# Performance work log

Measured on AMD Instinct MI355X. Metric: run time of the kernel, lower is better.

Reference implementation:

```python
import jax, jax.numpy as jnp
import numpy as np

B, N, E_PER = 512, 256, 8192          # graphs, nodes per graph, edges per graph
FIN, H, K, FOUT = 128, 32, 16, 10     # in_channels, hidden, num clusters, out_channels
EPS = 1e-15


def setup_inputs() -> dict:
    key = jax.random.key(0)
    ks = jax.random.split(key, 12)
    x = jax.random.normal(ks[0], (B * N, FIN), jnp.float32)
    # intra-graph random edges, then offset into the global node index space
    src = jax.random.randint(ks[1], (B, E_PER), 0, N)
    dst = jax.random.randint(ks[2], (B, E_PER), 0, N)
    offs = (jnp.arange(B) * N)[:, None]
    edge_index = jnp.stack([(src + offs).reshape(-1), (dst + offs).reshape(-1)]).astype(jnp.int64)
    batch = jnp.repeat(jnp.arange(B), N).astype(jnp.int64)

    def lin(k, fin, fout):
        return (jax.random.normal(k, (fin, fout), jnp.float32) / np.sqrt(fin)).astype(jnp.float32)

    params = {
        'W_lin1': lin(ks[3], FIN, H), 'b_lin1': jnp.zeros((H,), jnp.float32),
        'W_rel1': lin(ks[4], H, H), 'b_rel1': jnp.zeros((H,), jnp.float32),
        'W_root1': lin(ks[5], H, H),
        'W_pool': lin(ks[6], H, K), 'b_pool': jnp.zeros((K,), jnp.float32),
        'W_rel2': lin(ks[7], H, H), 'b_rel2': jnp.zeros((H,), jnp.float32),
        'W_root2': lin(ks[8], H, H),
        'W_lin2': lin(ks[9], H, H), 'b_lin2': jnp.zeros((H,), jnp.float32),
        'W_lin3': lin(ks[10], H, FOUT), 'b_lin3': jnp.zeros((FOUT,), jnp.float32),
    }
    return {'x': x, 'edge_index': edge_index, 'batch': batch, **params}


def _densify(x, edge_index, batch):
    """to_dense_adj + to_dense_batch: [total,F] -> [B,N,F], [B,N,N], [B,N]."""
    n_total = x.shape[0]
    counts = jax.ops.segment_sum(jnp.ones((n_total,), jnp.int32), batch, num_segments=B)
    offsets = jnp.concatenate([jnp.zeros((1,), jnp.int32), jnp.cumsum(counts)[:-1]])
    pos = jnp.arange(n_total) - offsets[batch]            # position of node inside its graph
    eb = batch[edge_index[0]]                             # graph id of each edge
    adj = jnp.zeros((B, N, N), jnp.float32).at[eb, pos[edge_index[0]], pos[edge_index[1]]].add(1.0)
    xd = jnp.zeros((B, N, x.shape[1]), jnp.float32).at[batch, pos].set(x)
    mask = jnp.zeros((B, N), jnp.float32).at[batch, pos].set(1.0)
    return xd, adj, mask


def _dense_graph_conv(x, adj, W_rel, b_rel, W_root):
    # PyG DenseGraphConv(aggr='add'): lin_rel(adj @ x) + lin_root(x)
    return jnp.einsum('bnm,bmh,hk->bnk', adj, x, W_rel) + b_rel + x @ W_root


def _dense_mincut_pool(x, adj, s, mask):
    s = jax.nn.softmax(s, axis=-1)
    x = x * mask[..., None]
    s = s * mask[..., None]
    out = jnp.einsum('bnk,bnh->bkh', s, x)                        # s^T x
    out_adj = jnp.einsum('bnk,bnm,bmj->bkj', s, adj, s)           # s^T A s
    mincut_num = jnp.einsum('bkk->b', out_adj)
    d_flat = adj.sum(-1)                                          # degree
    mincut_den = jnp.einsum('bnk,bn,bnk->b', s, d_flat, s)        # trace(s^T D s)
    mincut_loss = jnp.mean(-(mincut_num / mincut_den))
    ss = jnp.einsum('bnk,bnj->bkj', s, s)
    ss_norm = jnp.linalg.norm(ss, axis=(-1, -2), keepdims=True)
    i_s = jnp.eye(K, dtype=jnp.float32)
    ortho_loss = jnp.mean(jnp.linalg.norm(ss / ss_norm - i_s / jnp.sqrt(jnp.float32(K)), axis=(-1, -2)))
    # zero diagonal, symmetric degree normalization
    diag_mask = 1.0 - i_s
    out_adj = out_adj * diag_mask
    d = jnp.sqrt(out_adj.sum(-1))[:, None, :] + EPS               # [B,1,K]
    out_adj = out_adj / d / jnp.swapaxes(d, 1, 2)
    return out, out_adj, mincut_loss, ortho_loss


def reference(x, edge_index, batch, W_lin1, b_lin1, W_rel1, b_rel1, W_root1,
              W_pool, b_pool, W_rel2, b_rel2, W_root2, W_lin2, b_lin2, W_lin3, b_lin3):
    xd, adj, mask = _densify(x, edge_index, batch)
    h = xd @ W_lin1 + b_lin1                                      # lin1
    h = _dense_graph_conv(h, adj, W_rel1, b_rel1, W_root1)        # conv1
    s2 = h @ W_pool + b_pool                                      # pool2
    h, adj_p, mincut_loss2, ortho_loss2 = _dense_mincut_pool(h, adj, s2, mask)
    h = _dense_graph_conv(h, adj_p, W_rel2, b_rel2, W_root2)      # conv2
    h = h.sum(axis=1)                                             # readout sum over clusters
    h = jax.nn.relu(h @ W_lin2 + b_lin2)
    h = h @ W_lin3 + b_lin3
    return jax.nn.log_softmax(h, axis=-1), mincut_loss2, ortho_loss2
```

## Files before the change

kernel.cpp:

```cpp
#include <hip/hip_runtime.h>

#define NB 512
#define NN 256
#define EPG 8192
#define FINC 128

typedef float f32x4 __attribute__((ext_vector_type(4)));
typedef short s16x8 __attribute__((ext_vector_type(8)));

__device__ __forceinline__ float bf2f(unsigned short u) {
  union { unsigned int i; float f; } x; x.i = ((unsigned int)u) << 16; return x.f;
}
__device__ __forceinline__ unsigned short f2bf(float f) {
  union { float f; unsigned int i; } x; x.f = f;
  unsigned int r = x.i + 0x7fffu + ((x.i >> 16) & 1u);
  return (unsigned short)(r >> 16);
}
__device__ __forceinline__ unsigned pk2(unsigned short a, unsigned short c) {
  return (unsigned)a | ((unsigned)c << 16);
}

union U16x8 { uint4 u; s16x8 s; };
__device__ __forceinline__ s16x8 dec8(unsigned d) {
  U16x8 o;
  o.u.x = 0x41804180u | ((d & 0x0000000Fu) << 3)  | ((d & 0x000000F0u) << 15);
  o.u.y = 0x41804180u | ((d & 0x00000F00u) >> 5)  | ((d & 0x0000F000u) << 7);
  o.u.z = 0x41804180u | ((d & 0x000F0000u) >> 13) | ((d & 0x00F00000u) >> 1);
  o.u.w = 0x41804180u | ((d & 0x0F000000u) >> 21) | ((d & 0xF0000000u) >> 9);
  return o.s;
}

struct Params {
  const void* x; const void* ei;
  const void *wl1, *bl1, *wr1, *br1, *wro1, *wp, *bp;
  const void *wr2, *br2, *wro2, *wl2, *bl2, *wl3, *bl3;
  float* out; float* ws;
};

__device__ __forceinline__ bool detect_bf16(const void* p) {
  const unsigned short* pw = (const unsigned short*)p;
  int sane = 0;
  for (int i = 0; i < 64; ++i) {
    unsigned e = (pw[i] >> 7) & 0xFFu;
    sane += (e > 96u && e < 132u) ? 1 : 0;
  }
  return sane >= 56;
}
__device__ __forceinline__ bool detect_i64(const void* p) {
  const int* pi = (const int*)p + EPG;
  int ok = 0;
  for (int i = 0; i < 32; ++i) ok += (pi[i] >= 256 && pi[i] < 512) ? 1 : 0;
  return ok < 24;
}
__device__ __forceinline__ float ldf(const void* p, int i, bool bf) {
  return bf ? bf2f(((const unsigned short*)p)[i]) : ((const float*)p)[i];
}

#define SMEM_TOTAL 81920

__global__ __launch_bounds__(1024, 8) void mincut_main(Params P) {
  extern __shared__ char smem[];
  const int t = threadIdx.x;
  const int b = blockIdx.x;

  const bool BF  = detect_bf16(P.wr1);
  const bool I64 = detect_i64(P.ei);

  float* pbuf   = (float*)(smem + 0);
  float* oadjb  = (float*)(smem + 2048);
  float* ssb    = (float*)(smem + 3072);
  float* qbuf   = (float*)(smem + 4096);
  float* ddb    = (float*)(smem + 6144);
  float* h2b    = (float*)(smem + 6208);
  float* rb     = (float*)(smem + 8256);
  float* yb     = (float*)(smem + 8384);
  float* lgb    = (float*)(smem + 8512);
  float* scr    = (float*)(smem + 8704);
  float* rel2f  = (float*)(smem + 9216);
  float* root2f = (float*)(smem + 13312);
  float* lin2f  = (float*)(smem + 17408);
  float* lin3f  = (float*)(smem + 21504);
  float* brel2f = (float*)(smem + 22784);
  float* blin2f = (float*)(smem + 22912);
  float* blin3f = (float*)(smem + 23040);
  float* pbufH  = (float*)(smem + 24576);
  float* pbufL  = (float*)(smem + 26624);
  float* oadjH  = (float*)(smem + 28672);
  float* oadjL  = (float*)(smem + 29696);
  float* ssA    = (float*)(smem + 30720);
  float* ssX    = (float*)(smem + 31744);
  unsigned short* h0T  = (unsigned short*)(smem + 33792);
  unsigned short* h1Th = (unsigned short*)(smem + 33792);
  unsigned short* w1t  = (unsigned short*)(smem + 50688);
  unsigned short* zT   = (unsigned short*)(smem + 50688);
  unsigned short* sTh  = (unsigned short*)(smem + 50688);
  unsigned short* sTl  = (unsigned short*)(smem + 59136);
  unsigned short* wrelTh = (unsigned short*)(smem + 67584);
  unsigned short* wrelTl = (unsigned short*)(smem + 70144);
  unsigned short* wrootT = (unsigned short*)(smem + 72704);
  float* blin1f = (float*)(smem + 75264);
  unsigned short* taT = (unsigned short*)(smem + 67584);
  unsigned short* wpoolTh = (unsigned short*)(smem + 76032);
  unsigned short* wpoolTl = (unsigned short*)(smem + 77184);
  float*          colzF   = (float*)(smem + 78336);
  float*          colsF   = (float*)(smem + 78464);
  float*          scrE    = (float*)(smem + 78528);
  float*          bpf     = (float*)(smem + 78592);
  unsigned short* brel1h  = (unsigned short*)(smem + 81856);

  const int wv = t >> 6, lane = t & 63;
  const int lm = lane & 15, quad = lane >> 4;
  const int mbase = wv * 16;

  {
    uint4 z = {0u, 0u, 0u, 0u};
    for (int i = t; i < 2112; i += 1024) ((uint4*)smem)[i] = z;
  }
  if (t < 48) colzF[t] = 0.f;
  for (int e = t; e < 4096; e += 1024) {
    int k = e >> 5, c = e & 31;
    w1t[c * 136 + k] = f2bf(ldf(P.wl1, e, BF));
  }
  {
    int k = t >> 5, c = t & 31;
    float wr = ldf(P.wr1, t, BF);
    unsigned short hi = f2bf(wr);
    wrelTh[c * 40 + k] = hi;
    wrelTl[c * 40 + k] = f2bf(wr - bf2f(hi));
    wrootT[c * 40 + k] = f2bf(ldf(P.wro1, t, BF));
  }
  if (t < 512) {
    int m = t >> 4, c = t & 15;
    float w = ldf(P.wp, t, BF);
    unsigned short hi = f2bf(w);
    wpoolTh[c * 36 + m] = hi;
    wpoolTl[c * 36 + m] = f2bf(w - bf2f(hi));
  }
  if (t < 32) { blin1f[t] = ldf(P.bl1, t, BF); brel1h[t] = f2bf(ldf(P.br1, t, BF)); }
  if (t < 16) bpf[t] = ldf(P.bp, t, BF);
  __syncthreads();

  if (I64) {
    const uint4* s4 = (const uint4*)((const long long*)P.ei + (size_t)b * EPG) + t * 4;
    const uint4* d4 = (const uint4*)((const long long*)P.ei + (size_t)NB * EPG + (size_t)b * EPG) + t * 4;
    #pragma unroll
    for (int i = 0; i < 4; ++i) {
      uint4 a = s4[i], c = d4[i];
      unsigned n0 = (a.x & 255u) * 264u + (c.x & 255u);
      unsigned n1 = (a.z & 255u) * 264u + (c.z & 255u);
      atomicAdd((unsigned int*)(smem + ((n0 >> 3) << 2)), 1u << ((n0 & 7u) * 4u));
      atomicAdd((unsigned int*)(smem + ((n1 >> 3) << 2)), 1u << ((n1 & 7u) * 4u));
    }
  } else {
    const uint4* s4 = (const uint4*)((const int*)P.ei + (size_t)b * EPG) + t * 2;
    const uint4* d4 = (const uint4*)((const int*)P.ei + (size_t)NB * EPG + (size_t)b * EPG) + t * 2;
    #pragma unroll
    for (int i = 0; i < 2; ++i) {
      uint4 a = s4[i], c = d4[i];
      unsigned n0 = (a.x & 255u) * 264u + (c.x & 255u);
      unsigned n1 = (a.y & 255u) * 264u + (c.y & 255u);
      unsigned n2 = (a.z & 255u) * 264u + (c.z & 255u);
      unsigned n3 = (a.w & 255u) * 264u + (c.w & 255u);
      atomicAdd((unsigned int*)(smem + ((n0 >> 3) << 2)), 1u << ((n0 & 7u) * 4u));
      atomicAdd((unsigned int*)(smem + ((n1 >> 3) << 2)), 1u << ((n1 & 7u) * 4u));
      atomicAdd((unsigned int*)(smem + ((n2 >> 3) << 2)), 1u << ((n2 & 7u) * 4u));
      atomicAdd((unsigned int*)(smem + ((n3 >> 3) << 2)), 1u << ((n3 & 7u) * 4u));
    }
  }

  {
    f32x4 acc[2] = {{0.f,0.f,0.f,0.f},{0.f,0.f,0.f,0.f}};
    const size_t node = (size_t)(b * 256 + mbase + lm);
    #pragma unroll
    for (int ks = 0; ks < 4; ++ks) {
      const int k0 = ks * 32 + quad * 8;
      s16x8 a;
      if (BF) {
        a = *(const s16x8*)((const unsigned short*)P.x + node * 128 + k0);
      } else {
        const float* xp = (const float*)P.x + node * 128 + k0;
        f32x4 v0 = *(const f32x4*)xp;
        f32x4 v1 = *(const f32x4*)(xp + 4);
        #pragma unroll
        for (int j = 0; j < 4; ++j) { a[j] = (short)f2bf(v0[j]); a[4 + j] = (short)f2bf(v1[j]); }
      }
      #pragma unroll
      for (int ct = 0; ct < 2; ++ct) {
        s16x8 bh = *(const s16x8*)(w1t + (ct * 16 + lm) * 136 + k0);
        acc[ct] = __builtin_amdgcn_mfma_f32_16x16x32_bf16(a, bh, acc[ct], 0, 0, 0);
      }
    }
    #pragma unroll
    for (int ct = 0; ct < 2; ++ct) {
      const int c = ct * 16 + lm;
      float bias = blin1f[c];
      *(uint2*)(h0T + c * 264 + mbase + quad * 4) =
          make_uint2(pk2(f2bf(acc[ct][0] + bias), f2bf(acc[ct][1] + bias)),
                     pk2(f2bf(acc[ct][2] + bias), f2bf(acc[ct][3] + bias)));
    }
  }
  __syncthreads();

  f32x4 racc[2] = {{0.f,0.f,0.f,0.f},{0.f,0.f,0.f,0.f}};
  {
    s16x8 Ah;
    #pragma unroll
    for (int j = 0; j < 8; ++j) Ah[j] = (short)h0T[(quad * 8 + j) * 264 + mbase + lm];
    f32x4 zacc[2] = {{0.f,0.f,0.f,0.f},{0.f,0.f,0.f,0.f}};
    #pragma unroll
    for (int ct = 0; ct < 2; ++ct) {
      const int c = ct * 16 + lm;
      s16x8 brh = *(const s16x8*)(wrelTh + c * 40 + quad * 8);
      s16x8 brl = *(const s16x8*)(wrelTl + c * 40 + quad * 8);
      s16x8 bro = *(const s16x8*)(wrootT + c * 40 + quad * 8);
      zacc[ct] = __builtin_amdgcn_mfma_f32_16x16x32_bf16(Ah, brh, zacc[ct], 0, 0, 0);
      zacc[ct] = __builtin_amdgcn_mfma_f32_16x16x32_bf16(Ah, brl, zacc[ct], 0, 0, 0);
      racc[ct] = __builtin_amdgcn_mfma_f32_16x16x32_bf16(Ah, bro, racc[ct], 0, 0, 0);
    }
    #pragma unroll
    for (int ct = 0; ct < 2; ++ct) {
      unsigned short u0 = f2bf(zacc[ct][0]), u1 = f2bf(zacc[ct][1]);
      unsigned short u2 = f2bf(zacc[ct][2]), u3 = f2bf(zacc[ct][3]);
      *(uint2*)(zT + (ct * 16 + lm) * 264 + mbase + quad * 4) =
          make_uint2(pk2(u0, u1), pk2(u2, u3));
      float pz = (bf2f(u0) + bf2f(u1)) + (bf2f(u2) + bf2f(u3));
      pz += __shfl_xor(pz, 16, 64);
      pz += __shfl_xor(pz, 32, 64);
      if (lane < 16) atomicAdd(colzF + ct * 16 + lm, pz);
    }
  }
  __syncthreads();

  float degf;
  {
    f32x4 h1acc[2] = { racc[0], racc[1] };
    unsigned dsum = 0;
    const char* arow = smem + (mbase + lm) * 132;
    #pragma unroll
    for (int ks = 0; ks < 8; ++ks) {
      unsigned d = *(const unsigned int*)(arow + ks * 16 + quad * 4);
      unsigned v = (d & 0x0F0F0F0Fu) + ((d >> 4) & 0x0F0F0F0Fu);
      dsum += (v * 0x01010101u) >> 24;
      s16x8 af = dec8(d);
      const int v0 = ks * 32 + quad * 8;
      #pragma unroll
      for (int ct = 0; ct < 2; ++ct) {
        s16x8 bz = *(const s16x8*)(zT + (ct * 16 + lm) * 264 + v0);
        h1acc[ct] = __builtin_amdgcn_mfma_f32_16x16x32_bf16(af, bz, h1acc[ct], 0, 0, 0);
      }
    }
    dsum += __shfl_xor(dsum, 16, 64);
    dsum += __shfl_xor(dsum, 32, 64);
    degf = (float)dsum;
    #pragma unroll
    for (int ct = 0; ct < 2; ++ct) {
      const int c = ct * 16 + lm;
      float bias = bf2f(brel1h[c]) - 16.f * colzF[c];
      *(uint2*)(h1Th + c * 264 + mbase + quad * 4) =
          make_uint2(pk2(f2bf(h1acc[ct][0] + bias), f2bf(h1acc[ct][1] + bias)),
                     pk2(f2bf(h1acc[ct][2] + bias), f2bf(h1acc[ct][3] + bias)));
    }
  }
  __syncthreads();

  {
    s16x8 Ah1;
    #pragma unroll
    for (int j = 0; j < 8; ++j) Ah1[j] = (short)h1Th[(quad * 8 + j) * 264 + mbase + lm];
    s16x8 Bh, Bl;
    ((uint2*)&Bh)[0] = *(const uint2*)(wpoolTh + lm * 36 + quad * 8);
    ((uint2*)&Bh)[1] = *(const uint2*)(wpoolTh + lm * 36 + quad * 8 + 4);
    ((uint2*)&Bl)[0] = *(const uint2*)(wpoolTl + lm * 36 + quad * 8);
    ((uint2*)&Bl)[1] = *(const uint2*)(wpoolTl + lm * 36 + quad * 8 + 4);
    f32x4 lacc = {0.f, 0.f, 0.f, 0.f};
    lacc = __builtin_amdgcn_mfma_f32_16x16x32_bf16(Ah1, Bh, lacc, 0, 0, 0);
    lacc = __builtin_amdgcn_mfma_f32_16x16x32_bf16(Ah1, Bl, lacc, 0, 0, 0);
    f32x4 lg;
    float bm = bpf[lm];
    #pragma unroll
    for (int r = 0; r < 4; ++r) lg[r] = lacc[r] + bm;
    f32x4 mx = lg;
    #pragma unroll
    for (int m = 1; m <= 8; m <<= 1)
      #pragma unroll
      for (int r = 0; r < 4; ++r) mx[r] = fmaxf(mx[r], __shfl_xor(mx[r], m, 64));
    #pragma unroll
    for (int r = 0; r < 4; ++r) lg[r] = __expf(lg[r] - mx[r]);
    f32x4 sm = lg;
    #pragma unroll
    for (int m = 1; m <= 8; m <<= 1)
      #pragma unroll
      for (int r = 0; r < 4; ++r) sm[r] += __shfl_xor(sm[r], m, 64);
    f32x4 sval, sq;
    #pragma unroll
    for (int r = 0; r < 4; ++r) { sval[r] = lg[r] / sm[r]; sq[r] = sval[r] * sval[r]; }
    #pragma unroll
    for (int m = 1; m <= 8; m <<= 1)
      #pragma unroll
      for (int r = 0; r < 4; ++r) sq[r] += __shfl_xor(sq[r], m, 64);
    {
      unsigned short h0s = f2bf(sval[0]); float r0 = bf2f(h0s); unsigned short l0 = f2bf(sval[0] - r0);
      unsigned short h1s = f2bf(sval[1]); float r1 = bf2f(h1s); unsigned short l1 = f2bf(sval[1] - r1);
      unsigned short h2s = f2bf(sval[2]); float r2 = bf2f(h2s); unsigned short l2 = f2bf(sval[2] - r2);
      unsigned short h3s = f2bf(sval[3]); float r3 = bf2f(h3s); unsigned short l3 = f2bf(sval[3] - r3);
      const int nb = lm * 264 + mbase + quad * 4;
      *(uint2*)(sTh + nb) = make_uint2(pk2(h0s, h1s), pk2(h2s, h3s));
      *(uint2*)(sTl + nb) = make_uint2(pk2(l0, l1), pk2(l2, l3));
      float sr = ((r0 + bf2f(l0)) + (r1 + bf2f(l1))) + ((r2 + bf2f(l2)) + (r3 + bf2f(l3)));
      sr += __shfl_xor(sr, 16, 64);
      sr += __shfl_xor(sr, 32, 64);
      if (lane < 16) atomicAdd(colsF + lm, sr);
    }
    {
      int l = lane & 15, src = (l >> 2) << 4;
      float q0 = __shfl(sq[0], src, 64), q1 = __shfl(sq[1], src, 64);
      float q2 = __shfl(sq[2], src, 64), q3 = __shfl(sq[3], src, 64);
      float ssel = (l & 2) ? ((l & 1) ? q3 : q2) : ((l & 1) ? q1 : q0);
      float vden = (lane < 16) ? degf * ssel : 0.f;
      #pragma unroll
      for (int o = 32; o > 0; o >>= 1) vden += __shfl_xor(vden, o, 64);
      if (lane == 0) scrE[wv] = vden;
    }
  }
  __syncthreads();

  {
    float cols = colsF[lm];
    f32x4 tacc = {0.f, 0.f, 0.f, 0.f};
    const char* arow = smem + (mbase + lm) * 132;
    #pragma unroll
    for (int ks = 0; ks < 8; ++ks) {
      unsigned d = *(const unsigned int*)(arow + ks * 16 + quad * 4);
      s16x8 af = dec8(d);
      const int v0 = ks * 32 + quad * 8;
      s16x8 bh = *(const s16x8*)(sTh + lm * 264 + v0);
      s16x8 bl = *(const s16x8*)(sTl + lm * 264 + v0);
      tacc = __builtin_amdgcn_mfma_f32_16x16x32_bf16(af, bh, tacc, 0, 0, 0);
      tacc = __builtin_amdgcn_mfma_f32_16x16x32_bf16(af, bl, tacc, 0, 0, 0);
    }
    float c16 = 16.f * cols;
    *(uint2*)(taT + lm * 264 + mbase + quad * 4) =
        make_uint2(pk2(f2bf(tacc[0] - c16), f2bf(tacc[1] - c16)),
                   pk2(f2bf(tacc[2] - c16), f2bf(tacc[3] - c16)));
  }
  __syncthreads();

  rel2f[t] = ldf(P.wr2, t, BF);
  root2f[t] = ldf(P.wro2, t, BF);
  lin2f[t] = ldf(P.wl2, t, BF);
  if (t < 320) lin3f[t] = ldf(P.wl3, t, BF);
  if (t < 32) brel2f[t] = ldf(P.br2, t, BF);
  if (t < 32) blin2f[t] = ldf(P.bl2, t, BF);
  if (t < 10) blin3f[t] = ldf(P.bl3, t, BF);

  if (wv < 8) {
    const unsigned short *Ap, *Bp; float* dst; int W, ct = 0;
    switch (wv) {
      case 0: Ap = sTh; Bp = h1Th; dst = pbufH; W = 32; ct = 0; break;
      case 1: Ap = sTh; Bp = h1Th; dst = pbufH; W = 32; ct = 1; break;
      case 2: Ap = sTl; Bp = h1Th; dst = pbufL; W = 32; ct = 0; break;
      case 3: Ap = sTl; Bp = h1Th; dst = pbufL; W = 32; ct = 1; break;
      case 4: Ap = sTh; Bp = taT;  dst = oadjH; W = 16; break;
      case 5: Ap = sTl; Bp = taT;  dst = oadjL; W = 16; break;
      case 6: Ap = sTh; Bp = sTh;  dst = ssA;   W = 16; break;
      default: Ap = sTh; Bp = sTl; dst = ssX;   W = 16; break;
    }
    const int cidx = ct * 16 + lm;
    const unsigned short* Bb = Bp + cidx * 264;
    f32x4 acc = {0.f, 0.f, 0.f, 0.f};
    #pragma unroll
    for (int ch = 0; ch < 8; ++ch) {
      s16x8 a = *(const s16x8*)(Ap + lm * 264 + ch * 32 + quad * 8);
      s16x8 bb = *(const s16x8*)(Bb + ch * 32 + quad * 8);
      acc = __builtin_amdgcn_mfma_f32_16x16x32_bf16(a, bb, acc, 0, 0, 0);
    }
    #pragma unroll
    for (int r = 0; r < 4; ++r) dst[(quad * 4 + r) * W + cidx] = acc[r];
  }
  __syncthreads();

  if (t < 512) {
    pbuf[t] = pbufH[t] + pbufL[t];
  } else if (t < 768) {
    int i = t - 512; oadjb[i] = oadjH[i] + oadjL[i];
  } else {
    int i = t - 768; int k3 = i >> 4, j3 = i & 15;
    ssb[i] = ssA[i] + ssX[i] + ssX[j3 * 16 + k3];
  }
  __syncthreads();

  {
    float vnum = (t < 16) ? oadjb[t * 17] : 0.f;
    float vfro = (t < 256) ? ssb[t] * ssb[t] : 0.f;
    float vtr  = (t < 16) ? ssb[t * 17] : 0.f;
    #pragma unroll
    for (int o = 32; o > 0; o >>= 1) {
      vnum += __shfl_xor(vnum, o, 64);
      vfro += __shfl_xor(vfro, o, 64);
      vtr  += __shfl_xor(vtr, o, 64);
    }
    if (lane == 0) { scr[16 + wv] = vnum; scr[32 + wv] = vfro; scr[48 + wv] = vtr; }
  }
  __syncthreads();

  if (t == 0) {
    float den = 0.f, num = 0.f, fro = 0.f, tr = 0.f;
    #pragma unroll
    for (int i = 0; i < 16; ++i) { den += scrE[i]; num += scr[16 + i]; fro += scr[32 + i]; tr += scr[48 + i]; }
    float ssn = sqrtf(fro);
    float orth2 = 2.f - tr / (2.f * ssn);
    atomicAdd(P.ws, -(num / den) * (1.f / NB));
    atomicAdd(P.ws + 1, sqrtf(fmaxf(orth2, 0.f)) * (1.f / NB));
  }
  if (t < 16) {
    float rs = 0.f;
    #pragma unroll
    for (int j = 0; j < 16; ++j) if (j != t) rs += oadjb[t * 16 + j];
    ddb[t] = sqrtf(rs) + 1e-15f;
  }
  __syncthreads();
  if (t < 256) {
    int k = t >> 4, j = t & 15;
    float apv = (k == j) ? 0.f : oadjb[t] / (ddb[k] * ddb[j]);
    oadjb[t] = apv;
  }
  __syncthreads();

  if (t < 512) {
    int k = t >> 5, c = t & 31;
    float q = 0.f;
    #pragma unroll
    for (int j = 0; j < 16; ++j) q += oadjb[k * 16 + j] * pbuf[j * 32 + c];
    qbuf[k * 32 + c] = q;
  }
  __syncthreads();
  if (t < 512) {
    int k = t >> 5, c = t & 31;
    float s0 = 0.f;
    #pragma unroll
    for (int m = 0; m < 32; ++m)
      s0 += qbuf[k * 32 + m] * rel2f[m * 32 + c] + pbuf[k * 32 + m] * root2f[m * 32 + c];
    h2b[k * 32 + c] = s0;
  }
  __syncthreads();

  if (wv == 0) {
    if (lane < 32) {
      float r = 16.f * brel2f[lane];
      #pragma unroll
      for (int k = 0; k < 16; ++k) r += h2b[k * 32 + lane];
      rb[lane] = r;
    }
    if (lane < 32) {
      float y = blin2f[lane];
      #pragma unroll
      for (int m = 0; m < 32; ++m) y += rb[m] * lin2f[m * 32 + lane];
      yb[lane] = fmaxf(y, 0.f);
    }
    if (lane < 10) {
      float lg = blin3f[lane];
      #pragma unroll
      for (int m = 0; m < 32; ++m) lg += yb[m] * lin3f[m * 10 + lane];
      lgb[lane] = lg;
    }
    if (lane == 0) {
      float mx = lgb[0];
      #pragma unroll
      for (int i = 1; i < 10; ++i) mx = fmaxf(mx, lgb[i]);
      float sum = 0.f;
      #pragma unroll
      for (int i = 0; i < 10; ++i) sum += __expf(lgb[i] - mx);
      lgb[10] = mx + __logf(sum);
    }
    if (lane < 10) {
      float val = lgb[lane] - lgb[10];
      if (BF) ((unsigned short*)P.out)[b * 10 + lane] = f2bf(val);
      else    P.out[b * 10 + lane] = val;
    }
  }
}

__global__ void mincut_fin(Params P) {
  if (threadIdx.x == 0) {
    const bool BF = detect_bf16(P.wr1);
    if (BF) {
      ((unsigned short*)P.out)[5120] = f2bf(P.ws[0]);
      ((unsigned short*)P.out)[5121] = f2bf(P.ws[1]);
    } else {
      P.out[5120] = P.ws[0];
      P.out[5121] = P.ws[1];
    }
  }
}

extern "C" void kernel_launch(void* const* d_in, const int* in_sizes, int n_in,
                              void* d_out, int out_size, void* d_ws, size_t ws_size,
                              hipStream_t stream) {
  (void)in_sizes; (void)n_in; (void)out_size; (void)ws_size;
  Params P;
  P.x    = d_in[0];
  P.ei   = d_in[1];
  P.wl1  = d_in[3];
  P.bl1  = d_in[4];
  P.wr1  = d_in[5];
  P.br1  = d_in[6];
  P.wro1 = d_in[7];
  P.wp   = d_in[8];
  P.bp   = d_in[9];
  P.wr2  = d_in[10];
  P.br2  = d_in[11];
  P.wro2 = d_in[12];
  P.wl2  = d_in[13];
  P.bl2  = d_in[14];
  P.wl3  = d_in[15];
  P.bl3  = d_in[16];
  P.out  = (float*)d_out;
  P.ws   = (float*)d_ws;

  hipMemsetAsync(d_ws, 0, 2 * sizeof(float), stream);
  hipFuncSetAttribute(reinterpret_cast<const void*>(mincut_main),
                      hipFuncAttributeMaxDynamicSharedMemorySize, SMEM_TOTAL);
  hipLaunchKernelGGL(mincut_main, dim3(NB), dim3(1024), SMEM_TOTAL, stream, P);
  hipLaunchKernelGGL(mincut_fin, dim3(1), dim3(64), 0, stream, P);
}
```

Before: 170.1 us.

## Fold lin1 into conv1 weights and collapse pooled tail into single-wave reductions

```diff
diff --git a/kernel.cpp b/kernel.cpp
--- a/kernel.cpp
+++ b/kernel.cpp
@@ -66,16 +66,14 @@
   const bool BF  = detect_bf16(P.wr1);
   const bool I64 = detect_i64(P.ei);
 
-  float* pbuf   = (float*)(smem + 0);
   float* oadjb  = (float*)(smem + 2048);
-  float* ssb    = (float*)(smem + 3072);
-  float* qbuf   = (float*)(smem + 4096);
   float* ddb    = (float*)(smem + 6144);
-  float* h2b    = (float*)(smem + 6208);
+  float* caf    = (float*)(smem + 6208);
+  float* psf    = (float*)(smem + 6272);
+  float* qsf    = (float*)(smem + 6400);
   float* rb     = (float*)(smem + 8256);
   float* yb     = (float*)(smem + 8384);
   float* lgb    = (float*)(smem + 8512);
-  float* scr    = (float*)(smem + 8704);
   float* rel2f  = (float*)(smem + 9216);
   float* root2f = (float*)(smem + 13312);
   float* lin2f  = (float*)(smem + 17408);
@@ -89,24 +87,28 @@
   float* oadjL  = (float*)(smem + 29696);
   float* ssA    = (float*)(smem + 30720);
   float* ssX    = (float*)(smem + 31744);
-  unsigned short* h0T  = (unsigned short*)(smem + 33792);
-  unsigned short* h1Th = (unsigned short*)(smem + 33792);
-  unsigned short* w1t  = (unsigned short*)(smem + 50688);
-  unsigned short* zT   = (unsigned short*)(smem + 50688);
-  unsigned short* sTh  = (unsigned short*)(smem + 50688);
-  unsigned short* sTl  = (unsigned short*)(smem + 59136);
-  unsigned short* wrelTh = (unsigned short*)(smem + 67584);
-  unsigned short* wrelTl = (unsigned short*)(smem + 70144);
-  unsigned short* wrootT = (unsigned short*)(smem + 72704);
-  float* blin1f = (float*)(smem + 75264);
-  unsigned short* taT = (unsigned short*)(smem + 67584);
+  unsigned short* M_relTh = (unsigned short*)(smem + 33792);
+  unsigned short* M_relTl = (unsigned short*)(smem + 42240);
+  unsigned short* h1Th    = (unsigned short*)(smem + 33792);
+  unsigned short* w1t    = (unsigned short*)(smem + 50688);
+  unsigned short* wrelTh = (unsigned short*)(smem + 59392);
+  unsigned short* wrelTl = (unsigned short*)(smem + 61952);
+  unsigned short* wrootT = (unsigned short*)(smem + 64512);
+  float*          blin1f = (float*)(smem + 67072);
+  unsigned short* zT     = (unsigned short*)(smem + 50688);
+  unsigned short* sTh    = (unsigned short*)(smem + 50688);
+  unsigned short* sTl    = (unsigned short*)(smem + 59136);
+  unsigned short* M_rootTh = (unsigned short*)(smem + 67584);
+  unsigned short* taT      = (unsigned short*)(smem + 67584);
   unsigned short* wpoolTh = (unsigned short*)(smem + 76032);
   unsigned short* wpoolTl = (unsigned short*)(smem + 77184);
   float*          colzF   = (float*)(smem + 78336);
   float*          colsF   = (float*)(smem + 78464);
   float*          scrE    = (float*)(smem + 78528);
   float*          bpf     = (float*)(smem + 78592);
-  unsigned short* brel1h  = (unsigned short*)(smem + 81856);
+  float*          bzf     = (float*)(smem + 78656);
+  float*          brf     = (float*)(smem + 78784);
+  float*          brel1f  = (float*)(smem + 78912);
 
   const int wv = t >> 6, lane = t & 63;
   const int lm = lane & 15, quad = lane >> 4;
@@ -136,9 +138,28 @@
     wpoolTh[c * 36 + m] = hi;
     wpoolTl[c * 36 + m] = f2bf(w - bf2f(hi));
   }
-  if (t < 32) { blin1f[t] = ldf(P.bl1, t, BF); brel1h[t] = f2bf(ldf(P.br1, t, BF)); }
+  if (t < 32) { blin1f[t] = ldf(P.bl1, t, BF); brel1f[t] = ldf(P.br1, t, BF); }
   if (t < 16) bpf[t] = ldf(P.bp, t, BF);
   __syncthreads();
+
+  s16x8 xa[4];
+  {
+    const size_t node = (size_t)(b * 256 + mbase + lm);
+    if (BF) {
+      #pragma unroll
+      for (int ks = 0; ks < 4; ++ks)
+        xa[ks] = *(const s16x8*)((const unsigned short*)P.x + node * 128 + ks * 32 + quad * 8);
+    } else {
+      #pragma unroll
+      for (int ks = 0; ks < 4; ++ks) {
+        const float* xp = (const float*)P.x + node * 128 + ks * 32 + quad * 8;
+        f32x4 v0 = *(const f32x4*)xp;
+        f32x4 v1 = *(const f32x4*)(xp + 4);
+        #pragma unroll
+        for (int j = 0; j < 4; ++j) { xa[ks][j] = (short)f2bf(v0[j]); xa[ks][4 + j] = (short)f2bf(v1[j]); }
+      }
+    }
+  }
 
   if (I64) {
     const uint4* s4 = (const uint4*)((const long long*)P.ei + (size_t)b * EPG) + t * 4;
@@ -169,64 +190,75 @@
   }
 
   {
-    f32x4 acc[2] = {{0.f,0.f,0.f,0.f},{0.f,0.f,0.f,0.f}};
-    const size_t node = (size_t)(b * 256 + mbase + lm);
+    const int mt = wv & 7, ct2 = wv >> 3;
+    const int c = ct2 * 16 + lm;
+    s16x8 Aw;
+    #pragma unroll
+    for (int j = 0; j < 8; ++j)
+      Aw[j] = (short)w1t[(quad * 8 + j) * 136 + mt * 16 + lm];
+    s16x8 Brh = *(const s16x8*)(wrelTh + c * 40 + quad * 8);
+    s16x8 Brl = *(const s16x8*)(wrelTl + c * 40 + quad * 8);
+    s16x8 Bro = *(const s16x8*)(wrootT + c * 40 + quad * 8);
+    f32x4 mr = {0.f,0.f,0.f,0.f}, mo = {0.f,0.f,0.f,0.f};
+    mr = __builtin_amdgcn_mfma_f32_16x16x32_bf16(Aw, Brh, mr, 0, 0, 0);
+    mr = __builtin_amdgcn_mfma_f32_16x16x32_bf16(Aw, Brl, mr, 0, 0, 0);
+    mo = __builtin_amdgcn_mfma_f32_16x16x32_bf16(Aw, Bro, mo, 0, 0, 0);
+    unsigned short h0_ = f2bf(mr[0]), h1_ = f2bf(mr[1]);
+    unsigned short h2_ = f2bf(mr[2]), h3_ = f2bf(mr[3]);
+    const int base = c * 132 + mt * 16 + quad * 4;
+    *(uint2*)(M_relTh + base) = make_uint2(pk2(h0_, h1_), pk2(h2_, h3_));
+    *(uint2*)(M_relTl + base) = make_uint2(
+        pk2(f2bf(mr[0] - bf2f(h0_)), f2bf(mr[1] - bf2f(h1_))),
+        pk2(f2bf(mr[2] - bf2f(h2_)), f2bf(mr[3] - bf2f(h3_))));
+    *(uint2*)(M_rootTh + base) = make_uint2(
+        pk2(f2bf(mo[0]), f2bf(mo[1])), pk2(f2bf(mo[2]), f2bf(mo[3])));
+  }
+  if (wv == 0) {
+    if (lane < 32) {
+      float s = 0.f;
+      #pragma unroll 8
+      for (int m = 0; m < 32; ++m)
+        s += blin1f[m] * (bf2f(wrelTh[lane * 40 + m]) + bf2f(wrelTl[lane * 40 + m]));
+      bzf[lane] = s;
+    } else {
+      int c = lane - 32;
+      float s = brel1f[c];
+      #pragma unroll 8
+      for (int m = 0; m < 32; ++m)
+        s += blin1f[m] * bf2f(wrootT[c * 40 + m]);
+      brf[c] = s;
+    }
+  }
+  __syncthreads();
+
+  f32x4 racc[2] = {{0.f,0.f,0.f,0.f},{0.f,0.f,0.f,0.f}};
+  {
+    f32x4 zacc[2] = {{0.f,0.f,0.f,0.f},{0.f,0.f,0.f,0.f}};
     #pragma unroll
     for (int ks = 0; ks < 4; ++ks) {
       const int k0 = ks * 32 + quad * 8;
-      s16x8 a;
-      if (BF) {
-        a = *(const s16x8*)((const unsigned short*)P.x + node * 128 + k0);
-      } else {
-        const float* xp = (const float*)P.x + node * 128 + k0;
-        f32x4 v0 = *(const f32x4*)xp;
-        f32x4 v1 = *(const f32x4*)(xp + 4);
-        #pragma unroll
-        for (int j = 0; j < 4; ++j) { a[j] = (short)f2bf(v0[j]); a[4 + j] = (short)f2bf(v1[j]); }
-      }
       #pragma unroll
       for (int ct = 0; ct < 2; ++ct) {
-        s16x8 bh = *(const s16x8*)(w1t + (ct * 16 + lm) * 136 + k0);
-        acc[ct] = __builtin_amdgcn_mfma_f32_16x16x32_bf16(a, bh, acc[ct], 0, 0, 0);
+        const int c = ct * 16 + lm;
+        s16x8 bzh = *(const s16x8*)(M_relTh + c * 132 + k0);
+        s16x8 bzl = *(const s16x8*)(M_relTl + c * 132 + k0);
+        s16x8 bro = *(const s16x8*)(M_rootTh + c * 132 + k0);
+        zacc[ct] = __builtin_amdgcn_mfma_f32_16x16x32_bf16(xa[ks], bzh, zacc[ct], 0, 0, 0);
+        zacc[ct] = __builtin_amdgcn_mfma_f32_16x16x32_bf16(xa[ks], bzl, zacc[ct], 0, 0, 0);
+        racc[ct] = __builtin_amdgcn_mfma_f32_16x16x32_bf16(xa[ks], bro, racc[ct], 0, 0, 0);
       }
     }
     #pragma unroll
     for (int ct = 0; ct < 2; ++ct) {
       const int c = ct * 16 + lm;
-      float bias = blin1f[c];
-      *(uint2*)(h0T + c * 264 + mbase + quad * 4) =
-          make_uint2(pk2(f2bf(acc[ct][0] + bias), f2bf(acc[ct][1] + bias)),
-                     pk2(f2bf(acc[ct][2] + bias), f2bf(acc[ct][3] + bias)));
-    }
-  }
-  __syncthreads();
-
-  f32x4 racc[2] = {{0.f,0.f,0.f,0.f},{0.f,0.f,0.f,0.f}};
-  {
-    s16x8 Ah;
-    #pragma unroll
-    for (int j = 0; j < 8; ++j) Ah[j] = (short)h0T[(quad * 8 + j) * 264 + mbase + lm];
-    f32x4 zacc[2] = {{0.f,0.f,0.f,0.f},{0.f,0.f,0.f,0.f}};
-    #pragma unroll
-    for (int ct = 0; ct < 2; ++ct) {
-      const int c = ct * 16 + lm;
-      s16x8 brh = *(const s16x8*)(wrelTh + c * 40 + quad * 8);
-      s16x8 brl = *(const s16x8*)(wrelTl + c * 40 + quad * 8);
-      s16x8 bro = *(const s16x8*)(wrootT + c * 40 + quad * 8);
-      zacc[ct] = __builtin_amdgcn_mfma_f32_16x16x32_bf16(Ah, brh, zacc[ct], 0, 0, 0);
-      zacc[ct] = __builtin_amdgcn_mfma_f32_16x16x32_bf16(Ah, brl, zacc[ct], 0, 0, 0);
-      racc[ct] = __builtin_amdgcn_mfma_f32_16x16x32_bf16(Ah, bro, racc[ct], 0, 0, 0);
-    }
-    #pragma unroll
-    for (int ct = 0; ct < 2; ++ct) {
-      unsigned short u0 = f2bf(zacc[ct][0]), u1 = f2bf(zacc[ct][1]);
-      unsigned short u2 = f2bf(zacc[ct][2]), u3 = f2bf(zacc[ct][3]);
-      *(uint2*)(zT + (ct * 16 + lm) * 264 + mbase + quad * 4) =
-          make_uint2(pk2(u0, u1), pk2(u2, u3));
+      float bz = bzf[c];
+      unsigned short u0 = f2bf(zacc[ct][0] + bz), u1 = f2bf(zacc[ct][1] + bz);
+      unsigned short u2 = f2bf(zacc[ct][2] + bz), u3 = f2bf(zacc[ct][3] + bz);
+      *(uint2*)(zT + c * 264 + mbase + quad * 4) = make_uint2(pk2(u0, u1), pk2(u2, u3));
       float pz = (bf2f(u0) + bf2f(u1)) + (bf2f(u2) + bf2f(u3));
       pz += __shfl_xor(pz, 16, 64);
       pz += __shfl_xor(pz, 32, 64);
-      if (lane < 16) atomicAdd(colzF + ct * 16 + lm, pz);
+      if (lane < 16) atomicAdd(colzF + c, pz);
     }
   }
   __syncthreads();
@@ -255,7 +287,7 @@
     #pragma unroll
     for (int ct = 0; ct < 2; ++ct) {
       const int c = ct * 16 + lm;
-      float bias = bf2f(brel1h[c]) - 16.f * colzF[c];
+      float bias = brf[c] - 16.f * colzF[c];
       *(uint2*)(h1Th + c * 264 + mbase + quad * 4) =
           make_uint2(pk2(f2bf(h1acc[ct][0] + bias), f2bf(h1acc[ct][1] + bias)),
                      pk2(f2bf(h1acc[ct][2] + bias), f2bf(h1acc[ct][3] + bias)));
@@ -353,7 +385,7 @@
   if (t < 32) blin2f[t] = ldf(P.bl2, t, BF);
   if (t < 10) blin3f[t] = ldf(P.bl3, t, BF);
 
-  if (wv < 8) {
+  {
     const unsigned short *Ap, *Bp; float* dst; int W, ct = 0;
     switch (wv) {
       case 0: Ap = sTh; Bp = h1Th; dst = pbufH; W = 32; ct = 0; break;
@@ -365,90 +397,57 @@
       case 6: Ap = sTh; Bp = sTh;  dst = ssA;   W = 16; break;
       default: Ap = sTh; Bp = sTl; dst = ssX;   W = 16; break;
     }
-    const int cidx = ct * 16 + lm;
-    const unsigned short* Bb = Bp + cidx * 264;
-    f32x4 acc = {0.f, 0.f, 0.f, 0.f};
-    #pragma unroll
-    for (int ch = 0; ch < 8; ++ch) {
-      s16x8 a = *(const s16x8*)(Ap + lm * 264 + ch * 32 + quad * 8);
-      s16x8 bb = *(const s16x8*)(Bb + ch * 32 + quad * 8);
-      acc = __builtin_amdgcn_mfma_f32_16x16x32_bf16(a, bb, acc, 0, 0, 0);
-    }
-    #pragma unroll
-    for (int r = 0; r < 4; ++r) dst[(quad * 4 + r) * W + cidx] = acc[r];
-  }
-  __syncthreads();
-
-  if (t < 512) {
-    pbuf[t] = pbufH[t] + pbufL[t];
-  } else if (t < 768) {
-    int i = t - 512; oadjb[i] = oadjH[i] + oadjL[i];
-  } else {
-    int i = t - 768; int k3 = i >> 4, j3 = i & 15;
-    ssb[i] = ssA[i] + ssX[i] + ssX[j3 * 16 + k3];
-  }
-  __syncthreads();
-
-  {
-    float vnum = (t < 16) ? oadjb[t * 17] : 0.f;
-    float vfro = (t < 256) ? ssb[t] * ssb[t] : 0.f;
-    float vtr  = (t < 16) ? ssb[t * 17] : 0.f;
-    #pragma unroll
-    for (int o = 32; o > 0; o >>= 1) {
-      vnum += __shfl_xor(vnum, o, 64);
-      vfro += __shfl_xor(vfro, o, 64);
-      vtr  += __shfl_xor(vtr, o, 64);
-    }
-    if (lane == 0) { scr[16 + wv] = vnum; scr[32 + wv] = vfro; scr[48 + wv] = vtr; }
-  }
-  __syncthreads();
-
-  if (t == 0) {
-    float den = 0.f, num = 0.f, fro = 0.f, tr = 0.f;
-    #pragma unroll
-    for (int i = 0; i < 16; ++i) { den += scrE[i]; num += scr[16 + i]; fro += scr[32 + i]; tr += scr[48 + i]; }
-    float ssn = sqrtf(fro);
-    float orth2 = 2.f - tr / (2.f * ssn);
-    atomicAdd(P.ws, -(num / den) * (1.f / NB));
-    atomicAdd(P.ws + 1, sqrtf(fmaxf(orth2, 0.f)) * (1.f / NB));
-  }
-  if (t < 16) {
-    float rs = 0.f;
-    #pragma unroll
-    for (int j = 0; j < 16; ++j) if (j != t) rs += oadjb[t * 16 + j];
-    ddb[t] = sqrtf(rs) + 1e-15f;
-  }
-  __syncthreads();
-  if (t < 256) {
-    int k = t >> 4, j = t & 15;
-    float apv = (k == j) ? 0.f : oadjb[t] / (ddb[k] * ddb[j]);
-    oadjb[t] = apv;
-  }
-  __syncthreads();
-
-  if (t < 512) {
-    int k = t >> 5, c = t & 31;
-    float q = 0.f;
-    #pragma unroll
-    for (int j = 0; j < 16; ++j) q += oadjb[k * 16 + j] * pbuf[j * 32 + c];
-    qbuf[k * 32 + c] = q;
-  }
-  __syncthreads();
-  if (t < 512) {
-    int k = t >> 5, c = t & 31;
-    float s0 = 0.f;
-    #pragma unroll
-    for (int m = 0; m < 32; ++m)
-      s0 += qbuf[k * 32 + m] * rel2f[m * 32 + c] + pbuf[k * 32 + m] * root2f[m * 32 + c];
-    h2b[k * 32 + c] = s0;
+    if (wv < 8) {
+      const int cidx = ct * 16 + lm;
+      const unsigned short* Bb = Bp + cidx * 264;
+      f32x4 acc = {0.f, 0.f, 0.f, 0.f};
+      #pragma unroll
+      for (int ch = 0; ch < 8; ++ch) {
+        s16x8 a = *(const s16x8*)(Ap + lm * 264 + ch * 32 + quad * 8);
+        s16x8 bb = *(const s16x8*)(Bb + ch * 32 + quad * 8);
+        acc = __builtin_amdgcn_mfma_f32_16x16x32_bf16(a, bb, acc, 0, 0, 0);
+      }
+      #pragma unroll
+      for (int r = 0; r < 4; ++r) dst[(quad * 4 + r) * W + cidx] = acc[r];
+    }
   }
   __syncthreads();
 
   if (wv == 0) {
+    #pragma unroll
+    for (int u = 0; u < 4; ++u) {
+      int i = lane * 4 + u;
+      oadjb[i] = oadjH[i] + oadjL[i];
+    }
+    if (lane < 16) {
+      float rs = 0.f;
+      #pragma unroll
+      for (int j = 0; j < 16; ++j) if (j != lane) rs += oadjb[lane * 16 + j];
+      ddb[lane] = sqrtf(rs) + 1e-15f;
+    }
+    if (lane < 16) {
+      float s = 0.f;
+      float dj = ddb[lane];
+      #pragma unroll
+      for (int k = 0; k < 16; ++k)
+        if (k != lane) s += oadjb[k * 16 + lane] / (ddb[k] * dj);
+      caf[lane] = s;
+    }
+    if (lane < 32) {
+      float ps = 0.f, qs = 0.f;
+      #pragma unroll
+      for (int j = 0; j < 16; ++j) {
+        float pv = pbufH[j * 32 + lane] + pbufL[j * 32 + lane];
+        ps += pv;
+        qs += caf[j] * pv;
+      }
+      psf[lane] = ps; qsf[lane] = qs;
+    }
     if (lane < 32) {
       float r = 16.f * brel2f[lane];
       #pragma unroll
-      for (int k = 0; k < 16; ++k) r += h2b[k * 32 + lane];
+      for (int m = 0; m < 32; ++m)
+        r += qsf[m] * rel2f[m * 32 + lane] + psf[m] * root2f[m * 32 + lane];
       rb[lane] = r;
     }
     if (lane < 32) {
@@ -476,6 +475,30 @@
       float val = lgb[lane] - lgb[10];
       if (BF) ((unsigned short*)P.out)[b * 10 + lane] = f2bf(val);
       else    P.out[b * 10 + lane] = val;
+    }
+  } else if (wv == 1) {
+    float vfro = 0.f, vtr = 0.f;
+    #pragma unroll
+    for (int u = 0; u < 4; ++u) {
+      int i = lane * 4 + u, k = i >> 4, j = i & 15;
+      float ssv = ssA[i] + ssX[i] + ssX[j * 16 + k];
+      vfro += ssv * ssv;
+      if (k == j) vtr += ssv;
+    }
+    float vnum = (lane < 16) ? (oadjH[lane * 17] + oadjL[lane * 17]) : 0.f;
+    float vden = (lane < 16) ? scrE[lane] : 0.f;
+    #pragma unroll
+    for (int o = 32; o > 0; o >>= 1) {
+      vfro += __shfl_xor(vfro, o, 64);
+      vtr  += __shfl_xor(vtr, o, 64);
+      vnum += __shfl_xor(vnum, o, 64);
+      vden += __shfl_xor(vden, o, 64);
+    }
+    if (lane == 0) {
+      float ssn = sqrtf(vfro);
+      float orth2 = 2.f - vtr / (2.f * ssn);
+      atomicAdd(P.ws, -(vnum / vden) * (1.f / NB));
+      atomicAdd(P.ws + 1, sqrtf(fmaxf(orth2, 0.f)) * (1.f / NB));
     }
   }
 }
```

Result: slower. 187.8 us (+10.4%).

## Collapse post-pool tail algebraically into single-wave reductions, drop several block syncs

Applied to the files above, without the earlier changes.

```diff
diff --git a/kernel.cpp b/kernel.cpp
--- a/kernel.cpp
+++ b/kernel.cpp
@@ -63,19 +63,23 @@
   const int t = threadIdx.x;
   const int b = blockIdx.x;
 
-  const bool BF  = detect_bf16(P.wr1);
-  const bool I64 = detect_i64(P.ei);
-
-  float* pbuf   = (float*)(smem + 0);
+  int* flg = (int*)(smem + 78656);
+  if (t == 0) {
+    flg[0] = detect_bf16(P.wr1) ? 1 : 0;
+    flg[1] = detect_i64(P.ei) ? 1 : 0;
+  }
+  __syncthreads();
+  const bool BF  = (flg[0] != 0);
+  const bool I64 = (flg[1] != 0);
+
   float* oadjb  = (float*)(smem + 2048);
-  float* ssb    = (float*)(smem + 3072);
-  float* qbuf   = (float*)(smem + 4096);
   float* ddb    = (float*)(smem + 6144);
-  float* h2b    = (float*)(smem + 6208);
+  float* caf    = (float*)(smem + 6208);
+  float* psf    = (float*)(smem + 6272);
+  float* qsf    = (float*)(smem + 6400);
   float* rb     = (float*)(smem + 8256);
   float* yb     = (float*)(smem + 8384);
   float* lgb    = (float*)(smem + 8512);
-  float* scr    = (float*)(smem + 8704);
   float* rel2f  = (float*)(smem + 9216);
   float* root2f = (float*)(smem + 13312);
   float* lin2f  = (float*)(smem + 17408);
@@ -353,7 +357,7 @@
   if (t < 32) blin2f[t] = ldf(P.bl2, t, BF);
   if (t < 10) blin3f[t] = ldf(P.bl3, t, BF);
 
-  if (wv < 8) {
+  {
     const unsigned short *Ap, *Bp; float* dst; int W, ct = 0;
     switch (wv) {
       case 0: Ap = sTh; Bp = h1Th; dst = pbufH; W = 32; ct = 0; break;
@@ -365,90 +369,57 @@
       case 6: Ap = sTh; Bp = sTh;  dst = ssA;   W = 16; break;
       default: Ap = sTh; Bp = sTl; dst = ssX;   W = 16; break;
     }
-    const int cidx = ct * 16 + lm;
-    const unsigned short* Bb = Bp + cidx * 264;
-    f32x4 acc = {0.f, 0.f, 0.f, 0.f};
-    #pragma unroll
-    for (int ch = 0; ch < 8; ++ch) {
-      s16x8 a = *(const s16x8*)(Ap + lm * 264 + ch * 32 + quad * 8);
-      s16x8 bb = *(const s16x8*)(Bb + ch * 32 + quad * 8);
-      acc = __builtin_amdgcn_mfma_f32_16x16x32_bf16(a, bb, acc, 0, 0, 0);
-    }
-    #pragma unroll
-    for (int r = 0; r < 4; ++r) dst[(quad * 4 + r) * W + cidx] = acc[r];
-  }
-  __syncthreads();
-
-  if (t < 512) {
-    pbuf[t] = pbufH[t] + pbufL[t];
-  } else if (t < 768) {
-    int i = t - 512; oadjb[i] = oadjH[i] + oadjL[i];
-  } else {
-    int i = t - 768; int k3 = i >> 4, j3 = i & 15;
-    ssb[i] = ssA[i] + ssX[i] + ssX[j3 * 16 + k3];
-  }
-  __syncthreads();
-
-  {
-    float vnum = (t < 16) ? oadjb[t * 17] : 0.f;
-    float vfro = (t < 256) ? ssb[t] * ssb[t] : 0.f;
-    float vtr  = (t < 16) ? ssb[t * 17] : 0.f;
-    #pragma unroll
-    for (int o = 32; o > 0; o >>= 1) {
-      vnum += __shfl_xor(vnum, o, 64);
-      vfro += __shfl_xor(vfro, o, 64);
-      vtr  += __shfl_xor(vtr, o, 64);
-    }
-    if (lane == 0) { scr[16 + wv] = vnum; scr[32 + wv] = vfro; scr[48 + wv] = vtr; }
-  }
-  __syncthreads();
-
-  if (t == 0) {
-    float den = 0.f, num = 0.f, fro = 0.f, tr = 0.f;
-    #pragma unroll
-    for (int i = 0; i < 16; ++i) { den += scrE[i]; num += scr[16 + i]; fro += scr[32 + i]; tr += scr[48 + i]; }
-    float ssn = sqrtf(fro);
-    float orth2 = 2.f - tr / (2.f * ssn);
-    atomicAdd(P.ws, -(num / den) * (1.f / NB));
-    atomicAdd(P.ws + 1, sqrtf(fmaxf(orth2, 0.f)) * (1.f / NB));
-  }
-  if (t < 16) {
-    float rs = 0.f;
-    #pragma unroll
-    for (int j = 0; j < 16; ++j) if (j != t) rs += oadjb[t * 16 + j];
-    ddb[t] = sqrtf(rs) + 1e-15f;
-  }
-  __syncthreads();
-  if (t < 256) {
-    int k = t >> 4, j = t & 15;
-    float apv = (k == j) ? 0.f : oadjb[t] / (ddb[k] * ddb[j]);
-    oadjb[t] = apv;
-  }
-  __syncthreads();
-
-  if (t < 512) {
-    int k = t >> 5, c = t & 31;
-    float q = 0.f;
-    #pragma unroll
-    for (int j = 0; j < 16; ++j) q += oadjb[k * 16 + j] * pbuf[j * 32 + c];
-    qbuf[k * 32 + c] = q;
-  }
-  __syncthreads();
-  if (t < 512) {
-    int k = t >> 5, c = t & 31;
-    float s0 = 0.f;
-    #pragma unroll
-    for (int m = 0; m < 32; ++m)
-      s0 += qbuf[k * 32 + m] * rel2f[m * 32 + c] + pbuf[k * 32 + m] * root2f[m * 32 + c];
-    h2b[k * 32 + c] = s0;
+    if (wv < 8) {
+      const int cidx = ct * 16 + lm;
+      const unsigned short* Bb = Bp + cidx * 264;
+      f32x4 acc = {0.f, 0.f, 0.f, 0.f};
+      #pragma unroll
+      for (int ch = 0; ch < 8; ++ch) {
+        s16x8 a = *(const s16x8*)(Ap + lm * 264 + ch * 32 + quad * 8);
+        s16x8 bb = *(const s16x8*)(Bb + ch * 32 + quad * 8);
+        acc = __builtin_amdgcn_mfma_f32_16x16x32_bf16(a, bb, acc, 0, 0, 0);
+      }
+      #pragma unroll
+      for (int r = 0; r < 4; ++r) dst[(quad * 4 + r) * W + cidx] = acc[r];
+    }
   }
   __syncthreads();
 
   if (wv == 0) {
+    #pragma unroll
+    for (int u = 0; u < 4; ++u) {
+      int i = lane * 4 + u;
+      oadjb[i] = oadjH[i] + oadjL[i];
+    }
+    if (lane < 16) {
+      float rs = 0.f;
+      #pragma unroll
+      for (int j = 0; j < 16; ++j) if (j != lane) rs += oadjb[lane * 16 + j];
+      ddb[lane] = sqrtf(rs) + 1e-15f;
+    }
+    if (lane < 16) {
+      float s = 0.f;
+      float dj = ddb[lane];
+      #pragma unroll
+      for (int k = 0; k < 16; ++k)
+        if (k != lane) s += oadjb[k * 16 + lane] / (ddb[k] * dj);
+      caf[lane] = s;
+    }
+    if (lane < 32) {
+      float ps = 0.f, qs = 0.f;
+      #pragma unroll
+      for (int j = 0; j < 16; ++j) {
+        float pv = pbufH[j * 32 + lane] + pbufL[j * 32 + lane];
+        ps += pv;
+        qs += caf[j] * pv;
+      }
+      psf[lane] = ps; qsf[lane] = qs;
+    }
     if (lane < 32) {
       float r = 16.f * brel2f[lane];
       #pragma unroll
-      for (int k = 0; k < 16; ++k) r += h2b[k * 32 + lane];
+      for (int m = 0; m < 32; ++m)
+        r += qsf[m] * rel2f[m * 32 + lane] + psf[m] * root2f[m * 32 + lane];
       rb[lane] = r;
     }
     if (lane < 32) {
@@ -476,6 +447,30 @@
       float val = lgb[lane] - lgb[10];
       if (BF) ((unsigned short*)P.out)[b * 10 + lane] = f2bf(val);
       else    P.out[b * 10 + lane] = val;
+    }
+  } else if (wv == 1) {
+    float vfro = 0.f, vtr = 0.f;
+    #pragma unroll
+    for (int u = 0; u < 4; ++u) {
+      int i = lane * 4 + u, k = i >> 4, j = i & 15;
+      float ssv = ssA[i] + ssX[i] + ssX[j * 16 + k];
+      vfro += ssv * ssv;
+      if (k == j) vtr += ssv;
+    }
+    float vnum = (lane < 16) ? (oadjH[lane * 17] + oadjL[lane * 17]) : 0.f;
+    float vden = (lane < 16) ? scrE[lane] : 0.f;
+    #pragma unroll
+    for (int o = 32; o > 0; o >>= 1) {
+      vfro += __shfl_xor(vfro, o, 64);
+      vtr  += __shfl_xor(vtr, o, 64);
+      vnum += __shfl_xor(vnum, o, 64);
+      vden += __shfl_xor(vden, o, 64);
+    }
+    if (lane == 0) {
+      float ssn = sqrtf(vfro);
+      float orth2 = 2.f - vtr / (2.f * ssn);
+      atomicAdd(P.ws, -(vnum / vden) * (1.f / NB));
+      atomicAdd(P.ws + 1, sqrtf(fmaxf(orth2, 0.f)) * (1.f / NB));
     }
   }
 }
```

New measurement: 171.3 us. Within noise of the previous version (+0.7%).
